# Kernel optimization log

Hardware: AMD Instinct MI355X
Metric: run time of the kernel (lower is better)

## Reference

```python
import jax, jax.numpy as jnp
import numpy as np

B, T, E, U, V = 4096, 80, 100, 64, 10000

def setup_inputs() -> dict:
    key = jax.random.key(0)
    ks = jax.random.split(key, 10)
    s = lambda *sh: 0.05
    return {
        "tokens": jax.random.randint(ks[0], (B, T), 0, V, dtype=jnp.int32),
        "emb": jax.random.normal(ks[1], (V, E), jnp.float32) * 0.05,
        "k0": jax.random.normal(ks[2], (E, 4 * U), jnp.float32) * 0.05,
        "r0": jax.random.normal(ks[3], (U, 4 * U), jnp.float32) * 0.05,
        "b0": jnp.zeros((4 * U,), jnp.float32),
        "k1": jax.random.normal(ks[4], (E, 4 * U), jnp.float32) * 0.05,
        "r1": jax.random.normal(ks[5], (U, 4 * U), jnp.float32) * 0.05,
        "b1": jnp.zeros((4 * U,), jnp.float32),
        "Wd": jax.random.normal(ks[6], (U, 1), jnp.float32) * 0.05,
        "bd": jnp.zeros((1,), jnp.float32),
    }

def _lstm_cell(h, c, xt, k, r, b):
    # keras LSTMCell gate order: i, f, g(cell candidate), o
    z = xt @ k + h @ r + b  # [B, 4U]
    i, f, g, o = jnp.split(z, 4, axis=-1)
    c_new = jax.nn.sigmoid(f) * c + jax.nn.sigmoid(i) * jnp.tanh(g)
    h_new = jax.nn.sigmoid(o) * jnp.tanh(c_new)
    return h_new, c_new

def reference(tokens, emb, k0, r0, b0, k1, r1, b1, Wd, bd):
    x = emb[tokens]                 # [B, T, E]
    xs = jnp.swapaxes(x, 0, 1)      # [T, B, E] for scan over time
    zeros = jnp.zeros((tokens.shape[0], U), x.dtype)
    init = (zeros, zeros, zeros, zeros)  # h0, c0, h1, c1

    def step(state, xt):
        h0, c0, h1, c1 = state
        h0, c0 = _lstm_cell(h0, c0, xt, k0, r0, b0)
        # NOTE: original feeds the raw embedded word (not out0) to cell 1
        h1, c1 = _lstm_cell(h1, c1, xt, k1, r1, b1)
        return (h0, c0, h1, c1), None

    (h0, c0, h1, c1), _ = jax.lax.scan(step, init, xs)
    logits = h1 @ Wd + bd           # [B, 1]
    return jax.nn.sigmoid(logits)
```

## Files before the change

### kernel.cpp

```cpp
#include <hip/hip_runtime.h>
#include <hip/hip_bf16.h>
#include <stdint.h>

#define B_  4096
#define T_  80
#define E_  100
#define U_  64
#define G_  256
#define V_  10000

#define S_H  72
#define AS   136
#define KS2  132
#define TS   81
#define XS   260

typedef __attribute__((ext_vector_type(8))) __bf16 bf16x8;
typedef __attribute__((ext_vector_type(4))) __bf16 bf16x4;
typedef __attribute__((ext_vector_type(4))) float  floatx4;

__device__ __forceinline__ float sigmoidf_(float x) {
    return __builtin_amdgcn_rcpf(1.f + __expf(-x));
}

__device__ __forceinline__ float tanhf_(float x) {
    return fmaf(-2.f, __builtin_amdgcn_rcpf(__expf(2.f * x) + 1.f), 1.f);
}

__device__ __forceinline__ void gload16(const float* gsrc, const float* ldst) {
    __builtin_amdgcn_global_load_lds(
        (const __attribute__((address_space(1))) void*)(uintptr_t)gsrc,
        (__attribute__((address_space(3))) void*)(uintptr_t)ldst,
        16, 0, 0);
}

__global__ __launch_bounds__(256) void embk_kernel(const float* __restrict__ emb,
                                                   const float* __restrict__ k1,
                                                   const float* __restrict__ b1,
                                                   float* __restrict__ embk) {
    __shared__ __bf16 aLDS[64 * AS];
    __shared__ __bf16 kLDS[128 * KS2];

    const int tid  = threadIdx.x;
    const int lane = tid & 63;
    const int w    = tid >> 6;
    const int n    = lane & 15;
    const int kg   = lane >> 4;
    const int v0   = (blockIdx.x >> 1) * 64;
    const int n0   = (blockIdx.x & 1) * 128;
    const int nrows = min(64, V_ - v0);

    for (int i = tid; i < 64 * AS / 8; i += 256) {
        bf16x8 z;
#pragma unroll
        for (int jj = 0; jj < 8; ++jj) z[jj] = (__bf16)0.f;
        *(bf16x8*)(aLDS + i * 8) = z;
    }
    for (int i = tid; i < 28 * KS2; i += 256)
        kLDS[100 * KS2 + i] = (__bf16)0.f;

    const float bv0 = b1[n0 + w * 32 + n];
    const float bv1 = b1[n0 + w * 32 + 16 + n];

    __syncthreads();

    for (int i = tid; i < nrows * 25; i += 256) {
        int r = i / 25, q = i - r * 25;
        float4 ev = *(const float4*)(emb + (long)(v0 + r) * E_ + q * 4);
        bf16x4 bv; bv[0] = (__bf16)ev.x; bv[1] = (__bf16)ev.y;
                   bv[2] = (__bf16)ev.z; bv[3] = (__bf16)ev.w;
        *(bf16x4*)(aLDS + r * AS + q * 4) = bv;
    }
    for (int i = tid; i < 100 * 32; i += 256) {
        int k = i >> 5, cq = (i & 31) * 4;
        float4 kv = *(const float4*)(k1 + (long)k * G_ + n0 + cq);
        bf16x4 bv; bv[0] = (__bf16)kv.x; bv[1] = (__bf16)kv.y;
                   bv[2] = (__bf16)kv.z; bv[3] = (__bf16)kv.w;
        *(bf16x4*)(kLDS + k * KS2 + cq) = bv;
    }
    __syncthreads();

    bf16x8 bfr[2][4];
#pragma unroll
    for (int ct = 0; ct < 2; ++ct)
#pragma unroll
        for (int kc = 0; kc < 4; ++kc) {
            bf16x8 s;
#pragma unroll
            for (int jj = 0; jj < 8; ++jj)
                s[jj] = kLDS[(kc * 32 + kg * 8 + jj) * KS2 + w * 32 + ct * 16 + n];
            bfr[ct][kc] = s;
        }

#pragma unroll
    for (int mt = 0; mt < 4; ++mt) {
        const __bf16* ab = aLDS + (mt * 16 + n) * AS + kg * 8;
        bf16x8 a0 = *(const bf16x8*)(ab + 0);
        bf16x8 a1 = *(const bf16x8*)(ab + 32);
        bf16x8 a2 = *(const bf16x8*)(ab + 64);
        bf16x8 a3 = *(const bf16x8*)(ab + 96);
#pragma unroll
        for (int ct = 0; ct < 2; ++ct) {
            float bv = ct ? bv1 : bv0;
            floatx4 acc = {bv, bv, bv, bv};
            acc = __builtin_amdgcn_mfma_f32_16x16x32_bf16(a0, bfr[ct][0], acc, 0, 0, 0);
            acc = __builtin_amdgcn_mfma_f32_16x16x32_bf16(a1, bfr[ct][1], acc, 0, 0, 0);
            acc = __builtin_amdgcn_mfma_f32_16x16x32_bf16(a2, bfr[ct][2], acc, 0, 0, 0);
            acc = __builtin_amdgcn_mfma_f32_16x16x32_bf16(a3, bfr[ct][3], acc, 0, 0, 0);
#pragma unroll
            for (int r = 0; r < 4; ++r) {
                int v = v0 + mt * 16 + kg * 4 + r;
                if (v < V_) embk[(long)v * G_ + n0 + w * 32 + ct * 16 + n] = acc[r];
            }
        }
    }
}

template<int SEL, int RB, int WB>
__device__ __forceinline__ void lstm_step(
        int tt, int n, int kg, int w, int lane,
        const int* __restrict__ tokLDS,
        __bf16 (&hbuf)[2][16 * S_H],
        float (&xstage)[3][16 * XS],
        const bf16x8 (&afr)[4][2],
        const float* __restrict__ embk,
        float (&c)[4]) {
    const __bf16* hb = &hbuf[SEL ^ 1][0];
    bf16x8 hb0 = *(const bf16x8*)(hb + n * S_H + kg * 8);
    bf16x8 hb1 = *(const bf16x8*)(hb + n * S_H + 32 + kg * 8);
    const float* xrow = &xstage[RB][0] + n * XS + w * 16 + kg * 4;
    floatx4 a0 = *(const floatx4*)(xrow + 0);
    floatx4 a1 = *(const floatx4*)(xrow + 64);
    floatx4 a2 = *(const floatx4*)(xrow + 128);
    floatx4 a3 = *(const floatx4*)(xrow + 192);

#pragma unroll
    for (int j = 0; j < 4; ++j) {
        int tok = __builtin_amdgcn_readfirstlane(tokLDS[(w * 4 + j) * TS + tt]);
        gload16(embk + (long)tok * G_ + (lane << 2),
                &xstage[WB][0] + (w * 4 + j) * XS);
    }

    a0 = __builtin_amdgcn_mfma_f32_16x16x32_bf16(afr[0][0], hb0, a0, 0, 0, 0);
    a0 = __builtin_amdgcn_mfma_f32_16x16x32_bf16(afr[0][1], hb1, a0, 0, 0, 0);
    a1 = __builtin_amdgcn_mfma_f32_16x16x32_bf16(afr[1][0], hb0, a1, 0, 0, 0);
    a1 = __builtin_amdgcn_mfma_f32_16x16x32_bf16(afr[1][1], hb1, a1, 0, 0, 0);
    a2 = __builtin_amdgcn_mfma_f32_16x16x32_bf16(afr[2][0], hb0, a2, 0, 0, 0);
    a2 = __builtin_amdgcn_mfma_f32_16x16x32_bf16(afr[2][1], hb1, a2, 0, 0, 0);
    a3 = __builtin_amdgcn_mfma_f32_16x16x32_bf16(afr[3][0], hb0, a3, 0, 0, 0);
    a3 = __builtin_amdgcn_mfma_f32_16x16x32_bf16(afr[3][1], hb1, a3, 0, 0, 0);

    bf16x4 hv;
#pragma unroll
    for (int r = 0; r < 4; ++r) {
        float zi = a0[r], zf = a1[r], zg = a2[r], zo = a3[r];
        float cn = fmaf(sigmoidf_(zf), c[r], sigmoidf_(zi) * tanhf_(zg));
        float hn = sigmoidf_(zo) * tanhf_(cn);
        c[r] = cn;
        hv[r] = (__bf16)hn;
    }
    *(bf16x4*)(&hbuf[SEL][0] + n * S_H + w * 16 + kg * 4) = hv;

    asm volatile("s_waitcnt lgkmcnt(0) vmcnt(4)\n\ts_barrier" ::: "memory");
}

__global__ __launch_bounds__(256) void lstm_kernel(const int*   __restrict__ tokens,
                                                   const float* __restrict__ embk,
                                                   const float* __restrict__ r1,
                                                   const float* __restrict__ Wd,
                                                   const float* __restrict__ bd,
                                                   float* __restrict__ out) {
    __shared__ int    tokLDS[16 * TS];
    __shared__ __bf16 hbuf[2][16 * S_H];
    __shared__ float  xstage[3][16 * XS];

    const int tid  = threadIdx.x;
    const int lane = tid & 63;
    const int w    = tid >> 6;
    const int n    = lane & 15;
    const int kg   = lane >> 4;
    const int bb   = blockIdx.x * 16;

    for (int i = tid; i < 16 * T_; i += 256)
        tokLDS[(i / T_) * TS + (i % T_)] = tokens[bb * T_ + i];
    for (int i = tid; i < 2 * 16 * S_H; i += 256) (&hbuf[0][0])[i] = (__bf16)0.f;

    bf16x8 afr[4][2];
#pragma unroll
    for (int ct = 0; ct < 4; ++ct)
#pragma unroll
        for (int kc = 0; kc < 2; ++kc) {
            bf16x8 s;
#pragma unroll
            for (int jj = 0; jj < 8; ++jj)
                s[jj] = (__bf16)r1[(kc * 32 + kg * 8 + jj) * G_ + ct * 64 + w * 16 + n];
            afr[ct][kc] = s;
        }

    float c[4] = {0.f, 0.f, 0.f, 0.f};

    __syncthreads();

#pragma unroll
    for (int s = 0; s < 2; ++s)
#pragma unroll
        for (int j = 0; j < 4; ++j) {
            int tok = __builtin_amdgcn_readfirstlane(tokLDS[(w * 4 + j) * TS + s]);
            gload16(embk + (long)tok * G_ + (lane << 2),
                    &xstage[s][0] + (w * 4 + j) * XS);
        }
    asm volatile("s_waitcnt lgkmcnt(0) vmcnt(4)\n\ts_barrier" ::: "memory");

    for (int t = 0; t < 78; t += 6) {
        lstm_step<0, 0, 2>(t + 2, n, kg, w, lane, tokLDS, hbuf, xstage, afr, embk, c);
        lstm_step<1, 1, 0>(t + 3, n, kg, w, lane, tokLDS, hbuf, xstage, afr, embk, c);
        lstm_step<0, 2, 1>(t + 4, n, kg, w, lane, tokLDS, hbuf, xstage, afr, embk, c);
        lstm_step<1, 0, 2>(t + 5, n, kg, w, lane, tokLDS, hbuf, xstage, afr, embk, c);
        lstm_step<0, 1, 0>(t + 6, n, kg, w, lane, tokLDS, hbuf, xstage, afr, embk, c);
        lstm_step<1, 2, 1>(t + 7, n, kg, w, lane, tokLDS, hbuf, xstage, afr, embk, c);
    }
    lstm_step<0, 0, 2>(79, n, kg, w, lane, tokLDS, hbuf, xstage, afr, embk, c);
    lstm_step<1, 1, 0>(79, n, kg, w, lane, tokLDS, hbuf, xstage, afr, embk, c);

    asm volatile("s_waitcnt vmcnt(0)" ::: "memory");

    if (tid < 16) {
        const __bf16* hb = hbuf[1] + tid * S_H;
        float s = bd[0];
#pragma unroll
        for (int u = 0; u < U_; ++u) s = fmaf((float)hb[u], Wd[u], s);
        out[bb + tid] = sigmoidf_(s);
    }
}

extern "C" void kernel_launch(void* const* d_in, const int* in_sizes, int n_in,
                              void* d_out, int out_size, void* d_ws, size_t ws_size,
                              hipStream_t stream) {
    const int*   tokens = (const int*)  d_in[0];
    const float* emb    = (const float*)d_in[1];
    const float* k1     = (const float*)d_in[5];
    const float* r1     = (const float*)d_in[6];
    const float* b1     = (const float*)d_in[7];
    const float* Wd     = (const float*)d_in[8];
    const float* bd     = (const float*)d_in[9];
    float*       out    = (float*)d_out;

    float* embk = (float*)d_ws;

    embk_kernel<<<((V_ + 63) / 64) * 2, 256, 0, stream>>>(emb, k1, b1, embk);
    lstm_kernel<<<B_ / 16, 256, 0, stream>>>(tokens, embk, r1, Wd, bd, out);
}
```

Baseline: 137.9 us.

## Process 32 batch rows per LSTM block with two interleaved MFMA tiles

Each block now handles 32 batch rows instead of 16, so every wave computes two independent 16-row tiles per timestep. The two MFMA chains are interleaved, which hides MFMA latency and spreads the per-step barrier and serial recurrence cost over twice as many rows. In exchange the grid halves to 128 blocks on a 256-CU device, LDS use doubles, and register pressure rises. The token load also drops readfirstlane, so the gather address may become a per-lane value.

```diff
diff --git a/kernel.cpp b/kernel.cpp
--- a/kernel.cpp
+++ b/kernel.cpp
@@ -8,6 +8,8 @@
 #define U_  64
 #define G_  256
 #define V_  10000
+
+#define RPB 32
 
 #define S_H  72
 #define AS   136
@@ -120,48 +122,75 @@
 __device__ __forceinline__ void lstm_step(
         int tt, int n, int kg, int w, int lane,
         const int* __restrict__ tokLDS,
-        __bf16 (&hbuf)[2][16 * S_H],
-        float (&xstage)[3][16 * XS],
+        __bf16 (&hbuf)[2][RPB * S_H],
+        float (&xstage)[3][RPB * XS],
         const bf16x8 (&afr)[4][2],
         const float* __restrict__ embk,
-        float (&c)[4]) {
+        float (&c)[8]) {
     const __bf16* hb = &hbuf[SEL ^ 1][0];
-    bf16x8 hb0 = *(const bf16x8*)(hb + n * S_H + kg * 8);
-    bf16x8 hb1 = *(const bf16x8*)(hb + n * S_H + 32 + kg * 8);
-    const float* xrow = &xstage[RB][0] + n * XS + w * 16 + kg * 4;
-    floatx4 a0 = *(const floatx4*)(xrow + 0);
-    floatx4 a1 = *(const floatx4*)(xrow + 64);
-    floatx4 a2 = *(const floatx4*)(xrow + 128);
-    floatx4 a3 = *(const floatx4*)(xrow + 192);
+    bf16x8 hA0 = *(const bf16x8*)(hb + n * S_H + kg * 8);
+    bf16x8 hA1 = *(const bf16x8*)(hb + n * S_H + 32 + kg * 8);
+    bf16x8 hB0 = *(const bf16x8*)(hb + (16 + n) * S_H + kg * 8);
+    bf16x8 hB1 = *(const bf16x8*)(hb + (16 + n) * S_H + 32 + kg * 8);
+    const float* xrA = &xstage[RB][0] + n * XS + w * 16 + kg * 4;
+    const float* xrB = xrA + 16 * XS;
+    floatx4 a0 = *(const floatx4*)(xrA + 0);
+    floatx4 a1 = *(const floatx4*)(xrA + 64);
+    floatx4 a2 = *(const floatx4*)(xrA + 128);
+    floatx4 a3 = *(const floatx4*)(xrA + 192);
+    floatx4 b0 = *(const floatx4*)(xrB + 0);
+    floatx4 b1 = *(const floatx4*)(xrB + 64);
+    floatx4 b2 = *(const floatx4*)(xrB + 128);
+    floatx4 b3 = *(const floatx4*)(xrB + 192);
 
 #pragma unroll
     for (int j = 0; j < 4; ++j) {
-        int tok = __builtin_amdgcn_readfirstlane(tokLDS[(w * 4 + j) * TS + tt]);
-        gload16(embk + (long)tok * G_ + (lane << 2),
+        int tokA = tokLDS[(w * 4 + j) * TS + tt];
+        gload16(embk + (long)tokA * G_ + (lane << 2),
                 &xstage[WB][0] + (w * 4 + j) * XS);
-    }
-
-    a0 = __builtin_amdgcn_mfma_f32_16x16x32_bf16(afr[0][0], hb0, a0, 0, 0, 0);
-    a0 = __builtin_amdgcn_mfma_f32_16x16x32_bf16(afr[0][1], hb1, a0, 0, 0, 0);
-    a1 = __builtin_amdgcn_mfma_f32_16x16x32_bf16(afr[1][0], hb0, a1, 0, 0, 0);
-    a1 = __builtin_amdgcn_mfma_f32_16x16x32_bf16(afr[1][1], hb1, a1, 0, 0, 0);
-    a2 = __builtin_amdgcn_mfma_f32_16x16x32_bf16(afr[2][0], hb0, a2, 0, 0, 0);
-    a2 = __builtin_amdgcn_mfma_f32_16x16x32_bf16(afr[2][1], hb1, a2, 0, 0, 0);
-    a3 = __builtin_amdgcn_mfma_f32_16x16x32_bf16(afr[3][0], hb0, a3, 0, 0, 0);
-    a3 = __builtin_amdgcn_mfma_f32_16x16x32_bf16(afr[3][1], hb1, a3, 0, 0, 0);
-
-    bf16x4 hv;
+        int tokB = tokLDS[(16 + w * 4 + j) * TS + tt];
+        gload16(embk + (long)tokB * G_ + (lane << 2),
+                &xstage[WB][0] + (16 + w * 4 + j) * XS);
+    }
+
+    a0 = __builtin_amdgcn_mfma_f32_16x16x32_bf16(afr[0][0], hA0, a0, 0, 0, 0);
+    b0 = __builtin_amdgcn_mfma_f32_16x16x32_bf16(afr[0][0], hB0, b0, 0, 0, 0);
+    a0 = __builtin_amdgcn_mfma_f32_16x16x32_bf16(afr[0][1], hA1, a0, 0, 0, 0);
+    b0 = __builtin_amdgcn_mfma_f32_16x16x32_bf16(afr[0][1], hB1, b0, 0, 0, 0);
+    a1 = __builtin_amdgcn_mfma_f32_16x16x32_bf16(afr[1][0], hA0, a1, 0, 0, 0);
+    b1 = __builtin_amdgcn_mfma_f32_16x16x32_bf16(afr[1][0], hB0, b1, 0, 0, 0);
+    a1 = __builtin_amdgcn_mfma_f32_16x16x32_bf16(afr[1][1], hA1, a1, 0, 0, 0);
+    b1 = __builtin_amdgcn_mfma_f32_16x16x32_bf16(afr[1][1], hB1, b1, 0, 0, 0);
+    a2 = __builtin_amdgcn_mfma_f32_16x16x32_bf16(afr[2][0], hA0, a2, 0, 0, 0);
+    b2 = __builtin_amdgcn_mfma_f32_16x16x32_bf16(afr[2][0], hB0, b2, 0, 0, 0);
+    a2 = __builtin_amdgcn_mfma_f32_16x16x32_bf16(afr[2][1], hA1, a2, 0, 0, 0);
+    b2 = __builtin_amdgcn_mfma_f32_16x16x32_bf16(afr[2][1], hB1, b2, 0, 0, 0);
+    a3 = __builtin_amdgcn_mfma_f32_16x16x32_bf16(afr[3][0], hA0, a3, 0, 0, 0);
+    b3 = __builtin_amdgcn_mfma_f32_16x16x32_bf16(afr[3][0], hB0, b3, 0, 0, 0);
+    a3 = __builtin_amdgcn_mfma_f32_16x16x32_bf16(afr[3][1], hA1, a3, 0, 0, 0);
+    b3 = __builtin_amdgcn_mfma_f32_16x16x32_bf16(afr[3][1], hB1, b3, 0, 0, 0);
+
+    bf16x4 hvA, hvB;
 #pragma unroll
     for (int r = 0; r < 4; ++r) {
         float zi = a0[r], zf = a1[r], zg = a2[r], zo = a3[r];
         float cn = fmaf(sigmoidf_(zf), c[r], sigmoidf_(zi) * tanhf_(zg));
         float hn = sigmoidf_(zo) * tanhf_(cn);
         c[r] = cn;
-        hv[r] = (__bf16)hn;
-    }
-    *(bf16x4*)(&hbuf[SEL][0] + n * S_H + w * 16 + kg * 4) = hv;
-
-    asm volatile("s_waitcnt lgkmcnt(0) vmcnt(4)\n\ts_barrier" ::: "memory");
+        hvA[r] = (__bf16)hn;
+    }
+#pragma unroll
+    for (int r = 0; r < 4; ++r) {
+        float zi = b0[r], zf = b1[r], zg = b2[r], zo = b3[r];
+        float cn = fmaf(sigmoidf_(zf), c[4 + r], sigmoidf_(zi) * tanhf_(zg));
+        float hn = sigmoidf_(zo) * tanhf_(cn);
+        c[4 + r] = cn;
+        hvB[r] = (__bf16)hn;
+    }
+    *(bf16x4*)(&hbuf[SEL][0] + n * S_H + w * 16 + kg * 4) = hvA;
+    *(bf16x4*)(&hbuf[SEL][0] + (16 + n) * S_H + w * 16 + kg * 4) = hvB;
+
+    asm volatile("s_waitcnt lgkmcnt(0) vmcnt(8)\n\ts_barrier" ::: "memory");
 }
 
 __global__ __launch_bounds__(256) void lstm_kernel(const int*   __restrict__ tokens,
@@ -170,20 +199,20 @@
                                                    const float* __restrict__ Wd,
                                                    const float* __restrict__ bd,
                                                    float* __restrict__ out) {
-    __shared__ int    tokLDS[16 * TS];
-    __shared__ __bf16 hbuf[2][16 * S_H];
-    __shared__ float  xstage[3][16 * XS];
+    __shared__ int    tokLDS[RPB * TS];
+    __shared__ __bf16 hbuf[2][RPB * S_H];
+    __shared__ float  xstage[3][RPB * XS];
 
     const int tid  = threadIdx.x;
     const int lane = tid & 63;
     const int w    = tid >> 6;
     const int n    = lane & 15;
     const int kg   = lane >> 4;
-    const int bb   = blockIdx.x * 16;
-
-    for (int i = tid; i < 16 * T_; i += 256)
+    const int bb   = blockIdx.x * RPB;
+
+    for (int i = tid; i < RPB * T_; i += 256)
         tokLDS[(i / T_) * TS + (i % T_)] = tokens[bb * T_ + i];
-    for (int i = tid; i < 2 * 16 * S_H; i += 256) (&hbuf[0][0])[i] = (__bf16)0.f;
+    for (int i = tid; i < 2 * RPB * S_H; i += 256) (&hbuf[0][0])[i] = (__bf16)0.f;
 
     bf16x8 afr[4][2];
 #pragma unroll
@@ -197,7 +226,7 @@
             afr[ct][kc] = s;
         }
 
-    float c[4] = {0.f, 0.f, 0.f, 0.f};
+    float c[8] = {0.f, 0.f, 0.f, 0.f, 0.f, 0.f, 0.f, 0.f};
 
     __syncthreads();
 
@@ -205,11 +234,14 @@
     for (int s = 0; s < 2; ++s)
 #pragma unroll
         for (int j = 0; j < 4; ++j) {
-            int tok = __builtin_amdgcn_readfirstlane(tokLDS[(w * 4 + j) * TS + s]);
-            gload16(embk + (long)tok * G_ + (lane << 2),
+            int tokA = tokLDS[(w * 4 + j) * TS + s];
+            gload16(embk + (long)tokA * G_ + (lane << 2),
                     &xstage[s][0] + (w * 4 + j) * XS);
-        }
-    asm volatile("s_waitcnt lgkmcnt(0) vmcnt(4)\n\ts_barrier" ::: "memory");
+            int tokB = tokLDS[(16 + w * 4 + j) * TS + s];
+            gload16(embk + (long)tokB * G_ + (lane << 2),
+                    &xstage[s][0] + (16 + w * 4 + j) * XS);
+        }
+    asm volatile("s_waitcnt lgkmcnt(0) vmcnt(8)\n\ts_barrier" ::: "memory");
 
     for (int t = 0; t < 78; t += 6) {
         lstm_step<0, 0, 2>(t + 2, n, kg, w, lane, tokLDS, hbuf, xstage, afr, embk, c);
@@ -224,7 +256,7 @@
 
     asm volatile("s_waitcnt vmcnt(0)" ::: "memory");
 
-    if (tid < 16) {
+    if (tid < RPB) {
         const __bf16* hb = hbuf[1] + tid * S_H;
         float s = bd[0];
 #pragma unroll
@@ -248,5 +280,5 @@
     float* embk = (float*)d_ws;
 
     embk_kernel<<<((V_ + 63) / 64) * 2, 256, 0, stream>>>(emb, k1, b1, embk);
-    lstm_kernel<<<B_ / 16, 256, 0, stream>>>(tokens, embk, r1, Wd, bd, out);
-}
+    lstm_kernel<<<B_ / RPB, 256, 0, stream>>>(tokens, embk, r1, Wd, bd, out);
+}
```

Result: slower. 176.1 us (+27.7%).

## Halve batch rows per LSTM block to double grid size and occupancy

Applied to the files above, without the earlier changes.

Each block now handles 8 batch rows instead of 16, which doubles the number of blocks from 256 to 512 so more CUs are filled on the serial 80-step recurrence. The MFMA tile is still 16 wide, so rows are duplicated and each lane picks half of the accumulator results to compute 2 gate cells instead of 4. This halves the per-step elementwise work per lane and the embedding gathers per wave. The cost is that half the MFMA throughput goes to redundant rows, and readfirstlane is dropped on the token loads.

```diff
diff --git a/kernel.cpp b/kernel.cpp
--- a/kernel.cpp
+++ b/kernel.cpp
@@ -9,6 +9,8 @@
 #define G_  256
 #define V_  10000
 
+#define RPB 8
+
 #define S_H  72
 #define AS   136
 #define KS2  132
@@ -17,6 +19,7 @@
 
 typedef __attribute__((ext_vector_type(8))) __bf16 bf16x8;
 typedef __attribute__((ext_vector_type(4))) __bf16 bf16x4;
+typedef __attribute__((ext_vector_type(2))) __bf16 bf16x2;
 typedef __attribute__((ext_vector_type(4))) float  floatx4;
 
 __device__ __forceinline__ float sigmoidf_(float x) {
@@ -118,27 +121,27 @@
 
 template<int SEL, int RB, int WB>
 __device__ __forceinline__ void lstm_step(
-        int tt, int n, int kg, int w, int lane,
+        int tt, int n7, int hi, int kg, int w, int lane,
         const int* __restrict__ tokLDS,
-        __bf16 (&hbuf)[2][16 * S_H],
-        float (&xstage)[3][16 * XS],
+        __bf16 (&hbuf)[2][RPB * S_H],
+        float (&xstage)[3][RPB * XS],
         const bf16x8 (&afr)[4][2],
         const float* __restrict__ embk,
-        float (&c)[4]) {
+        float (&c)[2]) {
     const __bf16* hb = &hbuf[SEL ^ 1][0];
-    bf16x8 hb0 = *(const bf16x8*)(hb + n * S_H + kg * 8);
-    bf16x8 hb1 = *(const bf16x8*)(hb + n * S_H + 32 + kg * 8);
-    const float* xrow = &xstage[RB][0] + n * XS + w * 16 + kg * 4;
+    bf16x8 hb0 = *(const bf16x8*)(hb + n7 * S_H + kg * 8);
+    bf16x8 hb1 = *(const bf16x8*)(hb + n7 * S_H + 32 + kg * 8);
+    const float* xrow = &xstage[RB][0] + n7 * XS + w * 16 + kg * 4;
     floatx4 a0 = *(const floatx4*)(xrow + 0);
     floatx4 a1 = *(const floatx4*)(xrow + 64);
     floatx4 a2 = *(const floatx4*)(xrow + 128);
     floatx4 a3 = *(const floatx4*)(xrow + 192);
 
 #pragma unroll
-    for (int j = 0; j < 4; ++j) {
-        int tok = __builtin_amdgcn_readfirstlane(tokLDS[(w * 4 + j) * TS + tt]);
+    for (int j = 0; j < 2; ++j) {
+        int tok = tokLDS[(w * 2 + j) * TS + tt];
         gload16(embk + (long)tok * G_ + (lane << 2),
-                &xstage[WB][0] + (w * 4 + j) * XS);
+                &xstage[WB][0] + (w * 2 + j) * XS);
     }
 
     a0 = __builtin_amdgcn_mfma_f32_16x16x32_bf16(afr[0][0], hb0, a0, 0, 0, 0);
@@ -150,40 +153,49 @@
     a3 = __builtin_amdgcn_mfma_f32_16x16x32_bf16(afr[3][0], hb0, a3, 0, 0, 0);
     a3 = __builtin_amdgcn_mfma_f32_16x16x32_bf16(afr[3][1], hb1, a3, 0, 0, 0);
 
-    bf16x4 hv;
-#pragma unroll
-    for (int r = 0; r < 4; ++r) {
-        float zi = a0[r], zf = a1[r], zg = a2[r], zo = a3[r];
-        float cn = fmaf(sigmoidf_(zf), c[r], sigmoidf_(zi) * tanhf_(zg));
-        float hn = sigmoidf_(zo) * tanhf_(cn);
-        c[r] = cn;
-        hv[r] = (__bf16)hn;
-    }
-    *(bf16x4*)(&hbuf[SEL][0] + n * S_H + w * 16 + kg * 4) = hv;
-
-    asm volatile("s_waitcnt lgkmcnt(0) vmcnt(4)\n\ts_barrier" ::: "memory");
-}
-
-__global__ __launch_bounds__(256) void lstm_kernel(const int*   __restrict__ tokens,
-                                                   const float* __restrict__ embk,
-                                                   const float* __restrict__ r1,
-                                                   const float* __restrict__ Wd,
-                                                   const float* __restrict__ bd,
-                                                   float* __restrict__ out) {
-    __shared__ int    tokLDS[16 * TS];
-    __shared__ __bf16 hbuf[2][16 * S_H];
-    __shared__ float  xstage[3][16 * XS];
+    float zi0 = hi ? a0[2] : a0[0], zi1 = hi ? a0[3] : a0[1];
+    float zf0 = hi ? a1[2] : a1[0], zf1 = hi ? a1[3] : a1[1];
+    float zg0 = hi ? a2[2] : a2[0], zg1 = hi ? a2[3] : a2[1];
+    float zo0 = hi ? a3[2] : a3[0], zo1 = hi ? a3[3] : a3[1];
+
+    bf16x2 hv;
+    {
+        float cn = fmaf(sigmoidf_(zf0), c[0], sigmoidf_(zi0) * tanhf_(zg0));
+        float hn = sigmoidf_(zo0) * tanhf_(cn);
+        c[0] = cn; hv[0] = (__bf16)hn;
+    }
+    {
+        float cn = fmaf(sigmoidf_(zf1), c[1], sigmoidf_(zi1) * tanhf_(zg1));
+        float hn = sigmoidf_(zo1) * tanhf_(cn);
+        c[1] = cn; hv[1] = (__bf16)hn;
+    }
+    *(bf16x2*)(&hbuf[SEL][0] + n7 * S_H + w * 16 + kg * 4 + hi * 2) = hv;
+
+    asm volatile("s_waitcnt lgkmcnt(0) vmcnt(2)\n\ts_barrier" ::: "memory");
+}
+
+__global__ __launch_bounds__(256, 2) void lstm_kernel(const int*   __restrict__ tokens,
+                                                      const float* __restrict__ embk,
+                                                      const float* __restrict__ r1,
+                                                      const float* __restrict__ Wd,
+                                                      const float* __restrict__ bd,
+                                                      float* __restrict__ out) {
+    __shared__ int    tokLDS[RPB * TS];
+    __shared__ __bf16 hbuf[2][RPB * S_H];
+    __shared__ float  xstage[3][RPB * XS];
 
     const int tid  = threadIdx.x;
     const int lane = tid & 63;
     const int w    = tid >> 6;
     const int n    = lane & 15;
+    const int n7   = n & 7;
+    const int hi   = (n >> 3) & 1;
     const int kg   = lane >> 4;
-    const int bb   = blockIdx.x * 16;
-
-    for (int i = tid; i < 16 * T_; i += 256)
+    const int bb   = blockIdx.x * RPB;
+
+    for (int i = tid; i < RPB * T_; i += 256)
         tokLDS[(i / T_) * TS + (i % T_)] = tokens[bb * T_ + i];
-    for (int i = tid; i < 2 * 16 * S_H; i += 256) (&hbuf[0][0])[i] = (__bf16)0.f;
+    for (int i = tid; i < 2 * RPB * S_H; i += 256) (&hbuf[0][0])[i] = (__bf16)0.f;
 
     bf16x8 afr[4][2];
 #pragma unroll
@@ -197,34 +209,34 @@
             afr[ct][kc] = s;
         }
 
-    float c[4] = {0.f, 0.f, 0.f, 0.f};
+    float c[2] = {0.f, 0.f};
 
     __syncthreads();
 
 #pragma unroll
     for (int s = 0; s < 2; ++s)
 #pragma unroll
-        for (int j = 0; j < 4; ++j) {
-            int tok = __builtin_amdgcn_readfirstlane(tokLDS[(w * 4 + j) * TS + s]);
+        for (int j = 0; j < 2; ++j) {
+            int tok = tokLDS[(w * 2 + j) * TS + s];
             gload16(embk + (long)tok * G_ + (lane << 2),
-                    &xstage[s][0] + (w * 4 + j) * XS);
-        }
-    asm volatile("s_waitcnt lgkmcnt(0) vmcnt(4)\n\ts_barrier" ::: "memory");
+                    &xstage[s][0] + (w * 2 + j) * XS);
+        }
+    asm volatile("s_waitcnt lgkmcnt(0) vmcnt(2)\n\ts_barrier" ::: "memory");
 
     for (int t = 0; t < 78; t += 6) {
-        lstm_step<0, 0, 2>(t + 2, n, kg, w, lane, tokLDS, hbuf, xstage, afr, embk, c);
-        lstm_step<1, 1, 0>(t + 3, n, kg, w, lane, tokLDS, hbuf, xstage, afr, embk, c);
-        lstm_step<0, 2, 1>(t + 4, n, kg, w, lane, tokLDS, hbuf, xstage, afr, embk, c);
-        lstm_step<1, 0, 2>(t + 5, n, kg, w, lane, tokLDS, hbuf, xstage, afr, embk, c);
-        lstm_step<0, 1, 0>(t + 6, n, kg, w, lane, tokLDS, hbuf, xstage, afr, embk, c);
-        lstm_step<1, 2, 1>(t + 7, n, kg, w, lane, tokLDS, hbuf, xstage, afr, embk, c);
-    }
-    lstm_step<0, 0, 2>(79, n, kg, w, lane, tokLDS, hbuf, xstage, afr, embk, c);
-    lstm_step<1, 1, 0>(79, n, kg, w, lane, tokLDS, hbuf, xstage, afr, embk, c);
+        lstm_step<0, 0, 2>(t + 2, n7, hi, kg, w, lane, tokLDS, hbuf, xstage, afr, embk, c);
+        lstm_step<1, 1, 0>(t + 3, n7, hi, kg, w, lane, tokLDS, hbuf, xstage, afr, embk, c);
+        lstm_step<0, 2, 1>(t + 4, n7, hi, kg, w, lane, tokLDS, hbuf, xstage, afr, embk, c);
+        lstm_step<1, 0, 2>(t + 5, n7, hi, kg, w, lane, tokLDS, hbuf, xstage, afr, embk, c);
+        lstm_step<0, 1, 0>(t + 6, n7, hi, kg, w, lane, tokLDS, hbuf, xstage, afr, embk, c);
+        lstm_step<1, 2, 1>(t + 7, n7, hi, kg, w, lane, tokLDS, hbuf, xstage, afr, embk, c);
+    }
+    lstm_step<0, 0, 2>(79, n7, hi, kg, w, lane, tokLDS, hbuf, xstage, afr, embk, c);
+    lstm_step<1, 1, 0>(79, n7, hi, kg, w, lane, tokLDS, hbuf, xstage, afr, embk, c);
 
     asm volatile("s_waitcnt vmcnt(0)" ::: "memory");
 
-    if (tid < 16) {
+    if (tid < RPB) {
         const __bf16* hb = hbuf[1] + tid * S_H;
         float s = bd[0];
 #pragma unroll
@@ -248,5 +260,5 @@
     float* embk = (float*)d_ws;
 
     embk_kernel<<<((V_ + 63) / 64) * 2, 256, 0, stream>>>(emb, k1, b1, embk);
-    lstm_kernel<<<B_ / 16, 256, 0, stream>>>(tokens, embk, r1, Wd, bd, out);
-}
+    lstm_kernel<<<B_ / RPB, 256, 0, stream>>>(tokens, embk, r1, Wd, bd, out);
+}
```

Result: faster. 129.6 us (-6.0%).

## Give each wave its own batch rows to drop per-step block barriers

Applied to the files above, without the earlier changes.

The LSTM recurrence is repartitioned so that each wavefront owns four batch rows and computes all 256 gate columns for them, holding all 16 recurrent-weight fragments in registers. This removes the per-timestep s_barrier and the cross-wave hidden-state exchange through LDS. Each wave now runs 32 MFMAs per step in place of 8, and three quarters of each MFMA's output lanes go unused because only 4 of the 16 columns are real rows. Token prefetch moves into registers one step ahead, and the LDS strides change. The intent is to trade redundant MFMA work and higher register pressure (launch bounds now 256,1) for the removal of barrier latency on the serial timestep chain.

```diff
diff --git a/kernel.cpp b/kernel.cpp
--- a/kernel.cpp
+++ b/kernel.cpp
@@ -9,11 +9,11 @@
 #define G_  256
 #define V_  10000
 
-#define S_H  72
+#define S_H  80
 #define AS   136
 #define KS2  132
 #define TS   81
-#define XS   260
+#define XS   264
 
 typedef __attribute__((ext_vector_type(8))) __bf16 bf16x8;
 typedef __attribute__((ext_vector_type(4))) __bf16 bf16x4;
@@ -33,6 +33,8 @@
         (__attribute__((address_space(3))) void*)(uintptr_t)ldst,
         16, 0, 0);
 }
+
+#define MFMA16(A,B,C) __builtin_amdgcn_mfma_f32_16x16x32_bf16(A, B, C, 0, 0, 0)
 
 __global__ __launch_bounds__(256) void embk_kernel(const float* __restrict__ emb,
                                                    const float* __restrict__ k1,
@@ -103,10 +105,10 @@
         for (int ct = 0; ct < 2; ++ct) {
             float bv = ct ? bv1 : bv0;
             floatx4 acc = {bv, bv, bv, bv};
-            acc = __builtin_amdgcn_mfma_f32_16x16x32_bf16(a0, bfr[ct][0], acc, 0, 0, 0);
-            acc = __builtin_amdgcn_mfma_f32_16x16x32_bf16(a1, bfr[ct][1], acc, 0, 0, 0);
-            acc = __builtin_amdgcn_mfma_f32_16x16x32_bf16(a2, bfr[ct][2], acc, 0, 0, 0);
-            acc = __builtin_amdgcn_mfma_f32_16x16x32_bf16(a3, bfr[ct][3], acc, 0, 0, 0);
+            acc = MFMA16(a0, bfr[ct][0], acc);
+            acc = MFMA16(a1, bfr[ct][1], acc);
+            acc = MFMA16(a2, bfr[ct][2], acc);
+            acc = MFMA16(a3, bfr[ct][3], acc);
 #pragma unroll
             for (int r = 0; r < 4; ++r) {
                 int v = v0 + mt * 16 + kg * 4 + r;
@@ -116,120 +118,125 @@
     }
 }
 
-template<int SEL, int RB, int WB>
+template<int RS, int WS>
 __device__ __forceinline__ void lstm_step(
-        int tt, int n, int kg, int w, int lane,
-        const int* __restrict__ tokLDS,
-        __bf16 (&hbuf)[2][16 * S_H],
-        float (&xstage)[3][16 * XS],
-        const bf16x8 (&afr)[4][2],
+        int t, int lane, int n, int kg, int w, int m, int row,
+        const int* __restrict__ tokW, __bf16* hW, float* xst,
+        const bf16x8 (&afr)[16][2],
         const float* __restrict__ embk,
-        float (&c)[4]) {
-    const __bf16* hb = &hbuf[SEL ^ 1][0];
-    bf16x8 hb0 = *(const bf16x8*)(hb + n * S_H + kg * 8);
-    bf16x8 hb1 = *(const bf16x8*)(hb + n * S_H + 32 + kg * 8);
-    const float* xrow = &xstage[RB][0] + n * XS + w * 16 + kg * 4;
-    floatx4 a0 = *(const floatx4*)(xrow + 0);
-    floatx4 a1 = *(const floatx4*)(xrow + 64);
-    floatx4 a2 = *(const floatx4*)(xrow + 128);
-    floatx4 a3 = *(const floatx4*)(xrow + 192);
-
-#pragma unroll
-    for (int j = 0; j < 4; ++j) {
-        int tok = __builtin_amdgcn_readfirstlane(tokLDS[(w * 4 + j) * TS + tt]);
-        gload16(embk + (long)tok * G_ + (lane << 2),
-                &xstage[WB][0] + (w * 4 + j) * XS);
-    }
-
-    a0 = __builtin_amdgcn_mfma_f32_16x16x32_bf16(afr[0][0], hb0, a0, 0, 0, 0);
-    a0 = __builtin_amdgcn_mfma_f32_16x16x32_bf16(afr[0][1], hb1, a0, 0, 0, 0);
-    a1 = __builtin_amdgcn_mfma_f32_16x16x32_bf16(afr[1][0], hb0, a1, 0, 0, 0);
-    a1 = __builtin_amdgcn_mfma_f32_16x16x32_bf16(afr[1][1], hb1, a1, 0, 0, 0);
-    a2 = __builtin_amdgcn_mfma_f32_16x16x32_bf16(afr[2][0], hb0, a2, 0, 0, 0);
-    a2 = __builtin_amdgcn_mfma_f32_16x16x32_bf16(afr[2][1], hb1, a2, 0, 0, 0);
-    a3 = __builtin_amdgcn_mfma_f32_16x16x32_bf16(afr[3][0], hb0, a3, 0, 0, 0);
-    a3 = __builtin_amdgcn_mfma_f32_16x16x32_bf16(afr[3][1], hb1, a3, 0, 0, 0);
-
-    bf16x4 hv;
-#pragma unroll
-    for (int r = 0; r < 4; ++r) {
-        float zi = a0[r], zf = a1[r], zg = a2[r], zo = a3[r];
-        float cn = fmaf(sigmoidf_(zf), c[r], sigmoidf_(zi) * tanhf_(zg));
+        float (&c)[4], int (&tk)[4]) {
+    asm volatile("s_waitcnt vmcnt(4)" ::: "memory");
+
+    if (t + 2 < T_) {
+#pragma unroll
+        for (int r = 0; r < 4; ++r)
+            gload16(embk + (long)tk[r] * G_ + (lane << 2),
+                    xst + WS * (16 * XS) + (w * 4 + r) * XS);
+    }
+
+    const __bf16* hrow = hW + (w * 4 + row) * S_H;
+    bf16x8 hb0 = *(const bf16x8*)(hrow + kg * 8);
+    bf16x8 hb1 = *(const bf16x8*)(hrow + 32 + kg * 8);
+
+    if (t + 3 < T_) {
+#pragma unroll
+        for (int r = 0; r < 4; ++r)
+            tk[r] = tokW[(w * 4 + r) * TS + (t + 3)];
+    }
+
+    const float* xrow = xst + RS * (16 * XS) + (w * 4 + row) * XS + kg * 4;
+
+#pragma unroll
+    for (int ug = 0; ug < 4; ++ug) {
+        floatx4 ai = *(const floatx4*)(xrow + (ug +  0) * 16);
+        floatx4 af = *(const floatx4*)(xrow + (ug +  4) * 16);
+        floatx4 ag = *(const floatx4*)(xrow + (ug +  8) * 16);
+        floatx4 ao = *(const floatx4*)(xrow + (ug + 12) * 16);
+        ai = MFMA16(afr[ug +  0][0], hb0, ai); ai = MFMA16(afr[ug +  0][1], hb1, ai);
+        af = MFMA16(afr[ug +  4][0], hb0, af); af = MFMA16(afr[ug +  4][1], hb1, af);
+        ag = MFMA16(afr[ug +  8][0], hb0, ag); ag = MFMA16(afr[ug +  8][1], hb1, ag);
+        ao = MFMA16(afr[ug + 12][0], hb0, ao); ao = MFMA16(afr[ug + 12][1], hb1, ao);
+
+        float zi = (m & 2) ? ((m & 1) ? ai[3] : ai[2]) : ((m & 1) ? ai[1] : ai[0]);
+        float zf = (m & 2) ? ((m & 1) ? af[3] : af[2]) : ((m & 1) ? af[1] : af[0]);
+        float zg = (m & 2) ? ((m & 1) ? ag[3] : ag[2]) : ((m & 1) ? ag[1] : ag[0]);
+        float zo = (m & 2) ? ((m & 1) ? ao[3] : ao[2]) : ((m & 1) ? ao[1] : ao[0]);
+
+        float cn = fmaf(sigmoidf_(zf), c[ug], sigmoidf_(zi) * tanhf_(zg));
         float hn = sigmoidf_(zo) * tanhf_(cn);
-        c[r] = cn;
-        hv[r] = (__bf16)hn;
-    }
-    *(bf16x4*)(&hbuf[SEL][0] + n * S_H + w * 16 + kg * 4) = hv;
-
-    asm volatile("s_waitcnt lgkmcnt(0) vmcnt(4)\n\ts_barrier" ::: "memory");
-}
-
-__global__ __launch_bounds__(256) void lstm_kernel(const int*   __restrict__ tokens,
-                                                   const float* __restrict__ embk,
-                                                   const float* __restrict__ r1,
-                                                   const float* __restrict__ Wd,
-                                                   const float* __restrict__ bd,
-                                                   float* __restrict__ out) {
-    __shared__ int    tokLDS[16 * TS];
-    __shared__ __bf16 hbuf[2][16 * S_H];
-    __shared__ float  xstage[3][16 * XS];
+        c[ug] = cn;
+        hW[(w * 4 + row) * S_H + ug * 16 + kg * 4 + m] = (__bf16)hn;
+    }
+}
+
+__global__ __launch_bounds__(256, 1) void lstm_kernel(const int*   __restrict__ tokens,
+                                                      const float* __restrict__ embk,
+                                                      const float* __restrict__ r1,
+                                                      const float* __restrict__ Wd,
+                                                      const float* __restrict__ bd,
+                                                      float* __restrict__ out) {
+    __shared__ int    tokW[16 * TS];
+    __shared__ __bf16 hW[16 * S_H];
+    __shared__ float  xst[3 * 16 * XS];
 
     const int tid  = threadIdx.x;
     const int lane = tid & 63;
     const int w    = tid >> 6;
     const int n    = lane & 15;
+    const int row  = n & 3;
+    const int m    = n >> 2;
     const int kg   = lane >> 4;
     const int bb   = blockIdx.x * 16;
 
-    for (int i = tid; i < 16 * T_; i += 256)
-        tokLDS[(i / T_) * TS + (i % T_)] = tokens[bb * T_ + i];
-    for (int i = tid; i < 2 * 16 * S_H; i += 256) (&hbuf[0][0])[i] = (__bf16)0.f;
-
-    bf16x8 afr[4][2];
-#pragma unroll
-    for (int ct = 0; ct < 4; ++ct)
+    for (int i = lane; i < 4 * T_; i += 64) {
+        int r = i / T_, q = i - r * T_;
+        tokW[(w * 4 + r) * TS + q] = tokens[(long)(bb + w * 4 + r) * T_ + q];
+    }
+    for (int i = lane; i < 4 * S_H; i += 64)
+        hW[w * 4 * S_H + i] = (__bf16)0.f;
+
+    bf16x8 afr[16][2];
+#pragma unroll
+    for (int ct = 0; ct < 16; ++ct)
 #pragma unroll
         for (int kc = 0; kc < 2; ++kc) {
             bf16x8 s;
 #pragma unroll
             for (int jj = 0; jj < 8; ++jj)
-                s[jj] = (__bf16)r1[(kc * 32 + kg * 8 + jj) * G_ + ct * 64 + w * 16 + n];
+                s[jj] = (__bf16)r1[(kc * 32 + kg * 8 + jj) * G_ + ct * 16 + n];
             afr[ct][kc] = s;
         }
 
     float c[4] = {0.f, 0.f, 0.f, 0.f};
-
-    __syncthreads();
+    int tk[4];
 
 #pragma unroll
     for (int s = 0; s < 2; ++s)
 #pragma unroll
-        for (int j = 0; j < 4; ++j) {
-            int tok = __builtin_amdgcn_readfirstlane(tokLDS[(w * 4 + j) * TS + s]);
+        for (int r = 0; r < 4; ++r) {
+            int tok = tokW[(w * 4 + r) * TS + s];
             gload16(embk + (long)tok * G_ + (lane << 2),
-                    &xstage[s][0] + (w * 4 + j) * XS);
-        }
-    asm volatile("s_waitcnt lgkmcnt(0) vmcnt(4)\n\ts_barrier" ::: "memory");
-
-    for (int t = 0; t < 78; t += 6) {
-        lstm_step<0, 0, 2>(t + 2, n, kg, w, lane, tokLDS, hbuf, xstage, afr, embk, c);
-        lstm_step<1, 1, 0>(t + 3, n, kg, w, lane, tokLDS, hbuf, xstage, afr, embk, c);
-        lstm_step<0, 2, 1>(t + 4, n, kg, w, lane, tokLDS, hbuf, xstage, afr, embk, c);
-        lstm_step<1, 0, 2>(t + 5, n, kg, w, lane, tokLDS, hbuf, xstage, afr, embk, c);
-        lstm_step<0, 1, 0>(t + 6, n, kg, w, lane, tokLDS, hbuf, xstage, afr, embk, c);
-        lstm_step<1, 2, 1>(t + 7, n, kg, w, lane, tokLDS, hbuf, xstage, afr, embk, c);
-    }
-    lstm_step<0, 0, 2>(79, n, kg, w, lane, tokLDS, hbuf, xstage, afr, embk, c);
-    lstm_step<1, 1, 0>(79, n, kg, w, lane, tokLDS, hbuf, xstage, afr, embk, c);
+                    xst + s * (16 * XS) + (w * 4 + r) * XS);
+        }
+#pragma unroll
+    for (int r = 0; r < 4; ++r) tk[r] = tokW[(w * 4 + r) * TS + 2];
+
+    for (int t = 0; t < 78; t += 3) {
+        lstm_step<0, 2>(t,     lane, n, kg, w, m, row, tokW, hW, xst, afr, embk, c, tk);
+        lstm_step<1, 0>(t + 1, lane, n, kg, w, m, row, tokW, hW, xst, afr, embk, c, tk);
+        lstm_step<2, 1>(t + 2, lane, n, kg, w, m, row, tokW, hW, xst, afr, embk, c, tk);
+    }
+    lstm_step<0, 2>(78, lane, n, kg, w, m, row, tokW, hW, xst, afr, embk, c, tk);
+    lstm_step<1, 0>(79, lane, n, kg, w, m, row, tokW, hW, xst, afr, embk, c, tk);
 
     asm volatile("s_waitcnt vmcnt(0)" ::: "memory");
 
-    if (tid < 16) {
-        const __bf16* hb = hbuf[1] + tid * S_H;
+    if (lane < 4) {
+        const __bf16* hb = hW + (w * 4 + lane) * S_H;
         float s = bd[0];
 #pragma unroll
         for (int u = 0; u < U_; ++u) s = fmaf((float)hb[u], Wd[u], s);
-        out[bb + tid] = sigmoidf_(s);
+        out[bb + w * 4 + lane] = sigmoidf_(s);
     }
 }
 
```

New measurement: 158.0 us. 14.6% more time.
